# Performance work log

Measured on AMD Instinct MI355X. Metric: run time of the kernel, lower is better.

The kernel has to match this reference:

```python
import jax, jax.numpy as jnp
import numpy as np

B, S, E, H = 2, 2048, 2048, 8
D = E // H          # 256, also PMSNorm width
LAYER_IDX = 3
EPS = 1e-5
NEG = jnp.finfo(jnp.float32).min


def setup_inputs() -> dict:
    key = jax.random.key(0)
    k1, k2, k3 = jax.random.split(key, 3)
    return {
        "hidden_state": jax.random.normal(k1, (B, S, E), dtype=jnp.float32),
        "w_attn": jax.random.normal(k2, (E, 3 * E), dtype=jnp.float32) * 0.02,
        "w_proj": jax.random.normal(k3, (E, E), dtype=jnp.float32) * 0.02,
        "norm_weight": jnp.ones((D,), dtype=jnp.float32),
    }


def reference(hidden_state, w_attn, w_proj, norm_weight):
    # qkv projection (Linear, no bias): [B,S,3E]
    qkv = hidden_state @ w_attn
    q, k, v = jnp.split(qkv, 3, axis=-1)
    # split heads -> [B,H,S,D]
    q = q.reshape(B, S, H, D).transpose(0, 2, 1, 3)
    k = k.reshape(B, S, H, D).transpose(0, 2, 1, 3)
    v = v.reshape(B, S, H, D).transpose(0, 2, 1, 3)
    # scaled scores, extra layer-idx scaling as in the module
    scale = jnp.asarray(D, jnp.float32) ** 0.5 * (LAYER_IDX + 1)
    scores = jnp.einsum("bhqd,bhkd->bhqk", q, k) / scale
    # causal mask (tril buffer): masked positions -> float32 min
    causal = jnp.tril(jnp.ones((S, S), dtype=bool))
    scores = jnp.where(causal[None, None], scores, NEG)
    attn = jax.nn.softmax(scores, axis=-1)  # dropout is identity in eval
    o = jnp.einsum("bhqk,bhkd->bhqd", attn, v)
    # PMSNorm over last dim D (applied per-head, as in the source)
    o = o * jax.lax.rsqrt(jnp.mean(o * o, axis=-1, keepdims=True) + EPS)
    o = o * norm_weight
    # merge heads -> [B,S,E], output projection
    merged = o.transpose(0, 2, 1, 3).reshape(B, S, E)
    return merged @ w_proj
```

## Files before the change

### kernel.cpp

```cpp
#include <hip/hip_runtime.h>
#include <math.h>


typedef unsigned short u16;
typedef unsigned int   u32;
typedef u16   u16x8 __attribute__((ext_vector_type(8)));
typedef __bf16 bf16x8 __attribute__((ext_vector_type(8)));
typedef float f32x4 __attribute__((ext_vector_type(4)));

#define GPTR(p) ((const __attribute__((address_space(1))) void*)(p))
#define LPTR(p) ((__attribute__((address_space(3))) void*)(p))

__device__ __forceinline__ u16 f2bf(float x) {
  u32 u = __float_as_uint(x);
  return (u16)((u + 0x7fffu + ((u >> 16) & 1u)) >> 16);
}

__device__ __forceinline__ bf16x8 ld8(const void* p) {
  u16x8 v = *reinterpret_cast<const u16x8*>(p);
  return __builtin_bit_cast(bf16x8, v);
}

__device__ __forceinline__ void g2l16(const void* g, void* l) {
  __builtin_amdgcn_global_load_lds(GPTR(g), LPTR(l), 16, 0, 0);
}

__global__ void cast_bf16_kernel(const float* __restrict__ in, u16* __restrict__ out, int n8) {
  int i = blockIdx.x * 256 + threadIdx.x;
  if (i >= n8) return;
  const float4* p = reinterpret_cast<const float4*>(in) + (size_t)i * 2;
  float4 a = p[0], b = p[1];
  u16x8 v;
  v[0] = f2bf(a.x); v[1] = f2bf(a.y); v[2] = f2bf(a.z); v[3] = f2bf(a.w);
  v[4] = f2bf(b.x); v[5] = f2bf(b.y); v[6] = f2bf(b.z); v[7] = f2bf(b.w);
  reinterpret_cast<u16x8*>(out)[i] = v;
}

__global__ void tcast_kernel(const float* __restrict__ in, u16* __restrict__ out, int R, int C) {
  __shared__ float t[32][33];
  int bx = blockIdx.x * 32, by = blockIdx.y * 32;
  int x = threadIdx.x, y = threadIdx.y;
  #pragma unroll
  for (int k = 0; k < 32; k += 8)
    t[y + k][x] = in[(size_t)(by + y + k) * C + (bx + x)];
  __syncthreads();
  #pragma unroll
  for (int k = 0; k < 32; k += 8)
    out[(size_t)(bx + y + k) * R + (by + x)] = f2bf(t[x][y + k]);
}

__global__ void tv_kernel(const u16* __restrict__ qkv, u16* __restrict__ out) {
  __shared__ u16 t[32][33];
  int bh = blockIdx.z, b = bh >> 3, h = bh & 7;
  const u16* ip = qkv + (size_t)b * 2048 * 6144 + 4096 + h * 256;
  u16* op = out + (size_t)bh * 256 * 2048;
  int bx = blockIdx.x * 32, by = blockIdx.y * 32;
  int x = threadIdx.x, y = threadIdx.y;
  #pragma unroll
  for (int k = 0; k < 32; k += 8)
    t[y + k][x] = ip[(size_t)(by + y + k) * 6144 + (bx + x)];
  __syncthreads();
  #pragma unroll
  for (int k = 0; k < 32; k += 8)
    op[(size_t)(bx + y + k) * 2048 + (by + x)] = t[x][y + k];
}

__global__ __launch_bounds__(256) void gemm_bt_kernel(
    const u16* __restrict__ A, const u16* __restrict__ Bt,
    float* __restrict__ Cf, u16* __restrict__ Cb, int M, int N, int K) {
  __shared__ __align__(16) u16 sA[128 * 64];
  __shared__ __align__(16) u16 sB[128 * 64];
  const int tid = threadIdx.x;
  const int lane = tid & 63, w = tid >> 6;
  const int wr = w >> 1, wc = w & 1;
  const int g = lane >> 4, li = lane & 15;
  const int bn = blockIdx.x * 128, bm = blockIdx.y * 128;

  const char* aSrc[4]; const char* bSrc[4];
  char* aDst[4]; char* bDst[4];
  #pragma unroll
  for (int j = 0; j < 4; ++j) {
    int chunk = w * 4 + j;
    int o = chunk * 1024 + lane * 16;
    int row = o >> 7, cb = o & 127;
    int cbs = cb ^ ((row & 7) << 4);
    aSrc[j] = (const char*)A + (size_t)(bm + row) * K * 2 + cbs;
    bSrc[j] = (const char*)Bt + (size_t)(bn + row) * K * 2 + cbs;
    aDst[j] = (char*)sA + chunk * 1024;
    bDst[j] = (char*)sB + chunk * 1024;
  }
  const char* aRd[2][4]; const char* bRd[2][4];
  #pragma unroll
  for (int ks = 0; ks < 2; ++ks) {
    #pragma unroll
    for (int f = 0; f < 4; ++f) {
      int ra = wr * 64 + f * 16 + li;
      aRd[ks][f] = (const char*)sA + ra * 128 + ((ks * 64 + g * 16) ^ ((ra & 7) << 4));
      int rb = wc * 64 + f * 16 + li;
      bRd[ks][f] = (const char*)sB + rb * 128 + ((ks * 64 + g * 16) ^ ((rb & 7) << 4));
    }
  }

  const f32x4 fz = {0.f, 0.f, 0.f, 0.f};
  f32x4 acc[4][4];
  #pragma unroll
  for (int i = 0; i < 4; ++i)
    #pragma unroll
    for (int j = 0; j < 4; ++j) acc[i][j] = fz;

  for (int k0 = 0; k0 < K; k0 += 64) {
    #pragma unroll
    for (int j = 0; j < 4; ++j) { g2l16(aSrc[j], aDst[j]); g2l16(bSrc[j], bDst[j]); }
    #pragma unroll
    for (int j = 0; j < 4; ++j) { aSrc[j] += 128; bSrc[j] += 128; }
    __syncthreads();
    bf16x8 af[2][4], bfv[2][4];
    #pragma unroll
    for (int ks = 0; ks < 2; ++ks)
      #pragma unroll
      for (int f = 0; f < 4; ++f) { af[ks][f] = ld8(aRd[ks][f]); bfv[ks][f] = ld8(bRd[ks][f]); }
    #pragma unroll
    for (int ks = 0; ks < 2; ++ks)
      #pragma unroll
      for (int mf = 0; mf < 4; ++mf)
        #pragma unroll
        for (int nf = 0; nf < 4; ++nf)
          acc[mf][nf] = __builtin_amdgcn_mfma_f32_16x16x32_bf16(af[ks][mf], bfv[ks][nf], acc[mf][nf], 0, 0, 0);
    __syncthreads();
  }

  if (Cf) {
    #pragma unroll
    for (int mf = 0; mf < 4; ++mf)
      #pragma unroll
      for (int nf = 0; nf < 4; ++nf)
        #pragma unroll
        for (int r = 0; r < 4; ++r) {
          int gm = bm + wr * 64 + mf * 16 + g * 4 + r;
          int gn = bn + wc * 64 + nf * 16 + li;
          Cf[(size_t)gm * N + gn] = acc[mf][nf][r];
        }
  } else {
    #pragma unroll
    for (int mf = 0; mf < 4; ++mf)
      #pragma unroll
      for (int nf = 0; nf < 4; ++nf)
        #pragma unroll
        for (int r = 0; r < 4; ++r) {
          int gm = bm + wr * 64 + mf * 16 + g * 4 + r;
          int gn = bn + wc * 64 + nf * 16 + li;
          Cb[(size_t)gm * N + gn] = f2bf(acc[mf][nf][r]);
        }
  }
}

__global__ __launch_bounds__(512, 2) void attn_kernel(
    const u16* __restrict__ qkv, const u16* __restrict__ Vt,
    const float* __restrict__ nw, u16* __restrict__ Mrg) {
  __shared__ __align__(16) char smem[106496];
  char* sKb = smem;
  char* sVb = smem + 65536;
  char* sPb = smem + 65536 + 32768;
  float* oex  = (float*)smem;
  float* mlex = (float*)(smem + 65536);

  const int c = blockIdx.x;
  const int bh = c & 15, iu = c >> 4;
  const int b = bh >> 3, h = bh & 7;
  const int tid = threadIdx.x, lane = tid & 63, w = tid >> 6;
  const int kh = w >> 2, wq = w & 3;
  const int g = lane >> 4, li = lane & 15;
  const float MASKV = -30000.0f;
  const float MINIT = -1000.0f;
  const float isc = 1.0f / 64.0f;
  const f32x4 fz = {0.f, 0.f, 0.f, 0.f};
  const size_t KADV = (size_t)32 * 6144 * 2;

  #pragma unroll 1
  for (int uu = 0; uu < 2; ++uu) {
    const int qt = uu ? (31 - iu) : iu;
    const int nt = qt + 1;
    const int kvb0 = kh * nt * 32;

    int qrow = qt * 64 + wq * 16 + li;
    const u16* qp = qkv + (size_t)(b * 2048 + qrow) * 6144 + h * 256;
    bf16x8 qf[8];
    #pragma unroll
    for (int c8 = 0; c8 < 8; ++c8) qf[c8] = ld8(qp + c8 * 32 + g * 8);

    const char* kSrc[4]; u32 kDoff[4];
    #pragma unroll
    for (int j = 0; j < 4; ++j) {
      int chunk = wq * 4 + j;
      int o = chunk * 1024 + lane * 16;
      int row = o >> 9, cb = o & 511;
      int cbs = cb ^ ((row & 7) << 4);
      kSrc[j] = (const char*)qkv + ((size_t)(b * 2048 + kvb0 + row) * 6144 + 2048 + h * 256) * 2 + cbs;
      kDoff[j] = chunk * 1024;
    }
    const char* vSrc[4]; char* vDst[4];
    #pragma unroll
    for (int j = 0; j < 4; ++j) {
      int chunk = wq * 4 + j;
      int o = chunk * 1024 + lane * 16;
      int row = o >> 6, cb = o & 63;
      int cbs = cb ^ (((row >> 1) & 3) << 4);
      vSrc[j] = (const char*)Vt + ((size_t)(bh * 256 + row) * 2048 + kvb0) * 2 + cbs;
      vDst[j] = sVb + kh * 16384 + chunk * 1024;
    }

    f32x4 o_[16];
    #pragma unroll
    for (int nf = 0; nf < 16; ++nf) o_[nf] = fz;
    float m_[4] = {MINIT, MINIT, MINIT, MINIT};
    float l_[4] = {0.f, 0.f, 0.f, 0.f};

    {
      char* kb0 = sKb + (kh * 2 + 0) * 16384;
      #pragma unroll
      for (int j = 0; j < 4; ++j) { g2l16(kSrc[j], kb0 + kDoff[j]); kSrc[j] += KADV; }
    }
    asm volatile("s_waitcnt vmcnt(0)" ::: "memory");
    asm volatile("s_barrier" ::: "memory");

    int cur = 0;
    for (int t = 0; t < nt; ++t) {
      const bool more = (t < nt - 1);
      #pragma unroll
      for (int j = 0; j < 4; ++j) { g2l16(vSrc[j], vDst[j]); vSrc[j] += 64; }
      if (more) {
        char* kb = sKb + (kh * 2 + (cur ^ 1)) * 16384;
        #pragma unroll
        for (int j = 0; j < 4; ++j) { g2l16(kSrc[j], kb + kDoff[j]); kSrc[j] += KADV; }
      }

      f32x4 sacc[2];
      const char* kbase = sKb + (kh * 2 + cur) * 16384;
      __builtin_amdgcn_s_setprio(1);
      #pragma unroll
      for (int nf = 0; nf < 2; ++nf) {
        int row = nf * 16 + li;
        int swz = (row & 7) << 4;
        const char* kr = kbase + row * 512;
        f32x4 sa = fz, sb = fz;
        #pragma unroll
        for (int c8 = 0; c8 < 4; ++c8) {
          sa = __builtin_amdgcn_mfma_f32_16x16x32_bf16(qf[c8],     ld8(kr + ((c8 * 64 + g * 16) ^ swz)),       sa, 0, 0, 0);
          sb = __builtin_amdgcn_mfma_f32_16x16x32_bf16(qf[c8 + 4], ld8(kr + (((c8 + 4) * 64 + g * 16) ^ swz)), sb, 0, 0, 0);
        }
        sacc[nf] = sa + sb;
      }
      __builtin_amdgcn_s_setprio(0);

      const int tidx = kh * nt + t;
      const bool diag = (tidx >= 2 * qt);
      float p[2][4], m0[4];
      #pragma unroll
      for (int r = 0; r < 4; ++r) {
        int qr = qt * 64 + wq * 16 + g * 4 + r;
        float a0 = sacc[0][r] * isc;
        float a1 = sacc[1][r] * isc;
        if (diag) {
          if (tidx * 32 + li > qr) a0 = MASKV;
          if (tidx * 32 + 16 + li > qr) a1 = MASKV;
        }
        p[0][r] = a0; p[1][r] = a1;
        m0[r] = fmaxf(a0, a1);
      }
      bool need = (m0[0] > m_[0] + 8.f) || (m0[1] > m_[1] + 8.f) ||
                  (m0[2] > m_[2] + 8.f) || (m0[3] > m_[3] + 8.f);
      if (__any(need)) {
        #pragma unroll
        for (int r = 0; r < 4; ++r) {
          float mx = m0[r];
          mx = fmaxf(mx, __shfl_xor(mx, 1));
          mx = fmaxf(mx, __shfl_xor(mx, 2));
          mx = fmaxf(mx, __shfl_xor(mx, 4));
          mx = fmaxf(mx, __shfl_xor(mx, 8));
          float mn = fmaxf(m_[r], mx);
          float sc = __expf(m_[r] - mn);
          l_[r] *= sc; m_[r] = mn;
          #pragma unroll
          for (int nf = 0; nf < 16; ++nf) o_[nf][r] *= sc;
        }
      }
      #pragma unroll
      for (int r = 0; r < 4; ++r) {
        float e0 = __expf(p[0][r] - m_[r]);
        float e1 = __expf(p[1][r] - m_[r]);
        p[0][r] = e0; p[1][r] = e1;
        l_[r] += e0 + e1;
      }

      if (more) asm volatile("s_waitcnt vmcnt(4)" ::: "memory");
      else      asm volatile("s_waitcnt vmcnt(0)" ::: "memory");
      asm volatile("s_barrier" ::: "memory");

      char* sPw = sPb + kh * 4096 + wq * 1024;
      #pragma unroll
      for (int r = 0; r < 4; ++r) {
        int row = g * 4 + r;
        int swz = ((row >> 1) & 3) << 4;
        #pragma unroll
        for (int nf = 0; nf < 2; ++nf)
          *(u16*)(sPw + row * 64 + (((nf * 16 + li) * 2) ^ swz)) = f2bf(p[nf][r]);
      }
      asm volatile("s_waitcnt lgkmcnt(0)" ::: "memory");
      __builtin_amdgcn_sched_barrier(0);

      __builtin_amdgcn_s_setprio(1);
      {
        const char* vb = sVb + kh * 16384;
        bf16x8 pa = ld8(sPw + li * 64 + ((g * 16) ^ (((li >> 1) & 3) << 4)));
        #pragma unroll
        for (int nf = 0; nf < 16; ++nf) {
          int row = nf * 16 + li;
          bf16x8 vf = ld8(vb + row * 64 + ((g * 16) ^ (((row >> 1) & 3) << 4)));
          o_[nf] = __builtin_amdgcn_mfma_f32_16x16x32_bf16(pa, vf, o_[nf], 0, 0, 0);
        }
      }
      __builtin_amdgcn_s_setprio(0);

      asm volatile("s_barrier" ::: "memory");
      if (more) asm volatile("s_waitcnt vmcnt(0)" ::: "memory");
      cur ^= 1;
    }

    if (kh == 1) {
      #pragma unroll
      for (int nf = 0; nf < 16; ++nf)
        *(f32x4*)(oex + wq * 4096 + nf * 256 + lane * 4) = o_[nf];
      #pragma unroll
      for (int r = 0; r < 4; ++r) {
        mlex[wq * 512 + r * 64 + lane] = l_[r];
        mlex[wq * 512 + 256 + r * 64 + lane] = m_[r];
      }
    }
    __syncthreads();
    if (kh == 0) {
      float aw[4], bw[4], inv_l[4];
      #pragma unroll
      for (int r = 0; r < 4; ++r) {
        float mB = mlex[wq * 512 + 256 + r * 64 + lane];
        float lB = mlex[wq * 512 + r * 64 + lane];
        float mm = fmaxf(m_[r], mB);
        aw[r] = __expf(m_[r] - mm);
        bw[r] = __expf(mB - mm);
        float lr = l_[r] * aw[r] + lB * bw[r];
        lr += __shfl_xor(lr, 1);
        lr += __shfl_xor(lr, 2);
        lr += __shfl_xor(lr, 4);
        lr += __shfl_xor(lr, 8);
        inv_l[r] = 1.0f / lr;
      }
      #pragma unroll
      for (int nf = 0; nf < 16; ++nf) {
        f32x4 ob = *(f32x4*)(oex + wq * 4096 + nf * 256 + lane * 4);
        #pragma unroll
        for (int r = 0; r < 4; ++r)
          o_[nf][r] = o_[nf][r] * aw[r] + ob[r] * bw[r];
      }
      #pragma unroll
      for (int r = 0; r < 4; ++r) {
        float ss = 0.f;
        #pragma unroll
        for (int nf = 0; nf < 16; ++nf) {
          float v = o_[nf][r] * inv_l[r];
          ss += v * v;
        }
        ss += __shfl_xor(ss, 1);
        ss += __shfl_xor(ss, 2);
        ss += __shfl_xor(ss, 4);
        ss += __shfl_xor(ss, 8);
        float rms = rsqrtf(ss * (1.0f / 256.0f) + 1e-5f);
        int row = qt * 64 + wq * 16 + g * 4 + r;
        #pragma unroll
        for (int nf = 0; nf < 16; ++nf) {
          int d = nf * 16 + li;
          float v = o_[nf][r] * inv_l[r] * rms * nw[d];
          Mrg[((size_t)(b * 2048 + row)) * 2048 + h * 256 + d] = f2bf(v);
        }
      }
    }
    __syncthreads();
  }
}

extern "C" void kernel_launch(void* const* d_in, const int* in_sizes, int n_in,
                              void* d_out, int out_size, void* d_ws, size_t ws_size,
                              hipStream_t stream) {
  const float* hs  = (const float*)d_in[0];
  const float* wat = (const float*)d_in[1];
  const float* wpr = (const float*)d_in[2];
  const float* nw  = (const float*)d_in[3];
  float* out = (float*)d_out;

  char* ws = (char*)d_ws;
  u16* Xb   = (u16*)(ws + 0);
  u16* Wp_t = (u16*)(ws + (16u << 20));
  u16* Qkv  = (u16*)(ws + (24u << 20));
  u16* Vt   = (u16*)(ws + (72u << 20));
  u16* Mrg  = Xb;
  u16* Wa_t = (u16*)d_out;

  dim3 t328(32, 8);
  cast_bf16_kernel<<<4096, 256, 0, stream>>>(hs, Xb, 1048576);
  tcast_kernel<<<dim3(192, 64), t328, 0, stream>>>(wat, Wa_t, 2048, 6144);
  tcast_kernel<<<dim3(64, 64), t328, 0, stream>>>(wpr, Wp_t, 2048, 2048);
  gemm_bt_kernel<<<dim3(48, 32), 256, 0, stream>>>(Xb, Wa_t, nullptr, Qkv, 4096, 6144, 2048);
  tv_kernel<<<dim3(8, 64, 16), t328, 0, stream>>>(Qkv, Vt);
  attn_kernel<<<256, 512, 0, stream>>>(Qkv, Vt, nw, Mrg);
  gemm_bt_kernel<<<dim3(16, 32), 256, 0, stream>>>(Mrg, Wp_t, out, nullptr, 4096, 2048, 2048);
  (void)in_sizes; (void)n_in; (void)out_size; (void)ws_size;
}
```

Measured before the change: 268.9 us.

## Use 256x256 double-buffered GEMM tile for QKV projection

Adds a new GEMM kernel that computes a 256x256 output tile per 512-thread block. It double-buffers the LDS loads issued via global_load_lds, so the next K-slice is fetched while MFMA runs on the current one, and raises wave priority around the MFMA bursts. It replaces the 128x128 kernel for the QKV projection only, to improve data reuse and hide load latency. The cost is 128 KB of LDS per block and 384 blocks on 256 CUs, which gives a partial second wave and possible occupancy limits.

```diff
diff --git a/kernel.cpp b/kernel.cpp
--- a/kernel.cpp
+++ b/kernel.cpp
@@ -63,6 +63,122 @@
   #pragma unroll
   for (int k = 0; k < 32; k += 8)
     op[(size_t)(bx + y + k) * 2048 + (by + x)] = t[x][y + k];
+}
+
+__global__ __launch_bounds__(512, 2) void gemm256_kernel(
+    const u16* __restrict__ A, const u16* __restrict__ Bt,
+    float* __restrict__ Cf, u16* __restrict__ Cb, int M, int N, int K) {
+  __shared__ __align__(16) u16 sA[2][256 * 64];
+  __shared__ __align__(16) u16 sB[2][256 * 64];
+  const int tid = threadIdx.x;
+  const int lane = tid & 63, w = tid >> 6;
+  const int wr = w >> 2, wc = w & 3;
+  const int g = lane >> 4, li = lane & 15;
+  const int bn = blockIdx.x * 256, bm = blockIdx.y * 256;
+
+  const char* aSrc[4]; const char* bSrc[4]; u32 dOff[4];
+  #pragma unroll
+  for (int j = 0; j < 4; ++j) {
+    int chunk = w * 4 + j;
+    int o = chunk * 1024 + lane * 16;
+    int row = o >> 7;
+    int cbs = (o & 127) ^ ((row & 7) << 4);
+    aSrc[j] = (const char*)A + (size_t)(bm + row) * K * 2 + cbs;
+    bSrc[j] = (const char*)Bt + (size_t)(bn + row) * K * 2 + cbs;
+    dOff[j] = (u32)chunk * 1024;
+  }
+
+  const f32x4 fz = {0.f, 0.f, 0.f, 0.f};
+  f32x4 acc[8][4];
+  #pragma unroll
+  for (int i = 0; i < 8; ++i)
+    #pragma unroll
+    for (int j = 0; j < 4; ++j) acc[i][j] = fz;
+
+  const int NT = K >> 6;
+  #pragma unroll
+  for (int j = 0; j < 4; ++j) {
+    g2l16(aSrc[j], (char*)sA[0] + dOff[j]);
+    g2l16(bSrc[j], (char*)sB[0] + dOff[j]);
+    aSrc[j] += 128; bSrc[j] += 128;
+  }
+
+  for (int t = 0; t < NT; ++t) {
+    const int cur = t & 1;
+    const bool more = (t + 1 < NT);
+    asm volatile("s_barrier" ::: "memory");
+    if (more) {
+      #pragma unroll
+      for (int j = 0; j < 4; ++j) {
+        g2l16(aSrc[j], (char*)sA[cur ^ 1] + dOff[j]);
+        g2l16(bSrc[j], (char*)sB[cur ^ 1] + dOff[j]);
+        aSrc[j] += 128; bSrc[j] += 128;
+      }
+      asm volatile("s_waitcnt vmcnt(8)" ::: "memory");
+    } else {
+      asm volatile("s_waitcnt vmcnt(0)" ::: "memory");
+    }
+    asm volatile("s_barrier" ::: "memory");
+
+    const char* sAb = (const char*)sA[cur];
+    const char* sBb = (const char*)sB[cur];
+    bf16x8 bReg[2][4];
+    #pragma unroll
+    for (int nf = 0; nf < 4; ++nf) {
+      int rb = wc * 64 + nf * 16 + li;
+      int swz = (rb & 7) << 4;
+      const char* base = sBb + rb * 128;
+      bReg[0][nf] = ld8(base + ((g * 16) ^ swz));
+      bReg[1][nf] = ld8(base + ((64 + g * 16) ^ swz));
+    }
+    #pragma unroll
+    for (int q = 0; q < 4; ++q) {
+      bf16x8 aReg[2][2];
+      #pragma unroll
+      for (int sub = 0; sub < 2; ++sub) {
+        int ra = wr * 128 + (2 * q + sub) * 16 + li;
+        int swz = (ra & 7) << 4;
+        const char* base = sAb + ra * 128;
+        aReg[0][sub] = ld8(base + ((g * 16) ^ swz));
+        aReg[1][sub] = ld8(base + ((64 + g * 16) ^ swz));
+      }
+      __builtin_amdgcn_s_setprio(1);
+      #pragma unroll
+      for (int sub = 0; sub < 2; ++sub)
+        #pragma unroll
+        for (int nf = 0; nf < 4; ++nf)
+          #pragma unroll
+          for (int ks = 0; ks < 2; ++ks)
+            acc[2 * q + sub][nf] =
+                __builtin_amdgcn_mfma_f32_16x16x32_bf16(aReg[ks][sub], bReg[ks][nf],
+                                                        acc[2 * q + sub][nf], 0, 0, 0);
+      __builtin_amdgcn_s_setprio(0);
+    }
+  }
+
+  if (Cb) {
+    #pragma unroll
+    for (int mf = 0; mf < 8; ++mf)
+      #pragma unroll
+      for (int nf = 0; nf < 4; ++nf)
+        #pragma unroll
+        for (int r = 0; r < 4; ++r) {
+          int gm = bm + wr * 128 + mf * 16 + g * 4 + r;
+          int gn = bn + wc * 64 + nf * 16 + li;
+          Cb[(size_t)gm * N + gn] = f2bf(acc[mf][nf][r]);
+        }
+  } else {
+    #pragma unroll
+    for (int mf = 0; mf < 8; ++mf)
+      #pragma unroll
+      for (int nf = 0; nf < 4; ++nf)
+        #pragma unroll
+        for (int r = 0; r < 4; ++r) {
+          int gm = bm + wr * 128 + mf * 16 + g * 4 + r;
+          int gn = bn + wc * 64 + nf * 16 + li;
+          Cf[(size_t)gm * N + gn] = acc[mf][nf][r];
+        }
+  }
 }
 
 __global__ __launch_bounds__(256) void gemm_bt_kernel(
@@ -407,7 +523,7 @@
   cast_bf16_kernel<<<4096, 256, 0, stream>>>(hs, Xb, 1048576);
   tcast_kernel<<<dim3(192, 64), t328, 0, stream>>>(wat, Wa_t, 2048, 6144);
   tcast_kernel<<<dim3(64, 64), t328, 0, stream>>>(wpr, Wp_t, 2048, 2048);
-  gemm_bt_kernel<<<dim3(48, 32), 256, 0, stream>>>(Xb, Wa_t, nullptr, Qkv, 4096, 6144, 2048);
+  gemm256_kernel<<<dim3(24, 16), 512, 0, stream>>>(Xb, Wa_t, nullptr, Qkv, 4096, 6144, 2048);
   tv_kernel<<<dim3(8, 64, 16), t328, 0, stream>>>(Qkv, Vt);
   attn_kernel<<<256, 512, 0, stream>>>(Qkv, Vt, nw, Mrg);
   gemm_bt_kernel<<<dim3(16, 32), 256, 0, stream>>>(Mrg, Wp_t, out, nullptr, 4096, 2048, 2048);
```

New measurement: 278.6 us. 1.04x slower.

## Replace bf16 GEMM with 8-wave ping-pong pipelined kernel using larger tiles

Applied to the files above, without the earlier changes.

Replaces the simple 128x128 single-buffered GEMM with a templated 512-thread kernel that double-buffers LDS, splits each K-step into half-tiles, and interleaves async global-to-LDS loads with MFMA phases under explicit barriers, waitcnt and setprio. Tiles grow to 256x192 for the QKV projection and 256x128 for the output projection. The goal is to hide global load latency behind matrix math and raise arithmetic intensity. The hand-counted vmcnt values and dense barrier schedule are fragile, and the larger tiles cut the number of blocks.

```diff
diff --git a/kernel.cpp b/kernel.cpp
--- a/kernel.cpp
+++ b/kernel.cpp
@@ -65,93 +65,169 @@
     op[(size_t)(bx + y + k) * 2048 + (by + x)] = t[x][y + k];
 }
 
-__global__ __launch_bounds__(256) void gemm_bt_kernel(
+template<int WM, int WN, int MF, int NF, bool F32OUT>
+__global__ __launch_bounds__(512, 2) void gemm8p_kernel(
     const u16* __restrict__ A, const u16* __restrict__ Bt,
     float* __restrict__ Cf, u16* __restrict__ Cb, int M, int N, int K) {
-  __shared__ __align__(16) u16 sA[128 * 64];
-  __shared__ __align__(16) u16 sB[128 * 64];
-  const int tid = threadIdx.x;
-  const int lane = tid & 63, w = tid >> 6;
-  const int wr = w >> 1, wc = w & 1;
+  constexpr int BM = WM * MF * 16;
+  constexpr int BN = WN * NF * 16;
+  constexpr int BSTG = (BN * 128) / 8192;
+  constexpr int BBYTES = BN * 128;
+  __shared__ __align__(16) char smem[65536 + 2 * BBYTES];
+  char* sAb = smem;
+  char* sBb = smem + 65536;
+
+  const int tid = threadIdx.x, lane = tid & 63, w = tid >> 6;
+  const int wr = w / WN, wc = w % WN;
   const int g = lane >> 4, li = lane & 15;
-  const int bn = blockIdx.x * 128, bm = blockIdx.y * 128;
-
-  const char* aSrc[4]; const char* bSrc[4];
-  char* aDst[4]; char* bDst[4];
-  #pragma unroll
-  for (int j = 0; j < 4; ++j) {
-    int chunk = w * 4 + j;
-    int o = chunk * 1024 + lane * 16;
-    int row = o >> 7, cb = o & 127;
-    int cbs = cb ^ ((row & 7) << 4);
-    aSrc[j] = (const char*)A + (size_t)(bm + row) * K * 2 + cbs;
-    bSrc[j] = (const char*)Bt + (size_t)(bn + row) * K * 2 + cbs;
-    aDst[j] = (char*)sA + chunk * 1024;
-    bDst[j] = (char*)sB + chunk * 1024;
+  const int bn = blockIdx.x * BN, bm = blockIdx.y * BM;
+
+  const char* aS[2][2];
+  #pragma unroll
+  for (int h = 0; h < 2; ++h)
+    #pragma unroll
+    for (int j = 0; j < 2; ++j) {
+      int o = j * 8192 + tid * 16;
+      int row = o >> 6;
+      int col = (o & 63) ^ (((row >> 1) & 3) << 4);
+      aS[h][j] = (const char*)A + (size_t)(bm + row) * K * 2 + h * 64 + col;
+    }
+  const char* bS[BSTG];
+  #pragma unroll
+  for (int j = 0; j < BSTG; ++j) {
+    int o = j * 8192 + tid * 16;
+    int h = o / (BN * 64);
+    int rem = o - h * (BN * 64);
+    int row = rem >> 6;
+    int col = (rem & 63) ^ (((row >> 1) & 3) << 4);
+    bS[j] = (const char*)Bt + (size_t)(bn + row) * K * 2 + h * 64 + col;
   }
-  const char* aRd[2][4]; const char* bRd[2][4];
-  #pragma unroll
-  for (int ks = 0; ks < 2; ++ks) {
-    #pragma unroll
-    for (int f = 0; f < 4; ++f) {
-      int ra = wr * 64 + f * 16 + li;
-      aRd[ks][f] = (const char*)sA + ra * 128 + ((ks * 64 + g * 16) ^ ((ra & 7) << 4));
-      int rb = wc * 64 + f * 16 + li;
-      bRd[ks][f] = (const char*)sB + rb * 128 + ((ks * 64 + g * 16) ^ ((rb & 7) << 4));
-    }
+
+  u32 aRd[MF], bRd[NF];
+  #pragma unroll
+  for (int mf = 0; mf < MF; ++mf) {
+    int row = wr * (MF * 16) + mf * 16 + li;
+    aRd[mf] = row * 64 + ((g * 16) ^ (((row >> 1) & 3) << 4));
   }
+  #pragma unroll
+  for (int nf = 0; nf < NF; ++nf) {
+    int row = wc * (NF * 16) + nf * 16 + li;
+    bRd[nf] = row * 64 + ((g * 16) ^ (((row >> 1) & 3) << 4));
+  }
+
+  auto stageA = [&](int h, int buf) {
+    char* d = sAb + (buf * 2 + h) * 16384 + w * 1024;
+    g2l16(aS[h][0], d);
+    g2l16(aS[h][1], d + 8192);
+    aS[h][0] += 128; aS[h][1] += 128;
+  };
+  auto stageB = [&](int buf) {
+    char* d = sBb + buf * BBYTES + w * 1024;
+    #pragma unroll
+    for (int j = 0; j < BSTG; ++j) { g2l16(bS[j], d + j * 8192); bS[j] += 128; }
+  };
 
   const f32x4 fz = {0.f, 0.f, 0.f, 0.f};
-  f32x4 acc[4][4];
-  #pragma unroll
-  for (int i = 0; i < 4; ++i)
-    #pragma unroll
-    for (int j = 0; j < 4; ++j) acc[i][j] = fz;
-
-  for (int k0 = 0; k0 < K; k0 += 64) {
-    #pragma unroll
-    for (int j = 0; j < 4; ++j) { g2l16(aSrc[j], aDst[j]); g2l16(bSrc[j], bDst[j]); }
-    #pragma unroll
-    for (int j = 0; j < 4; ++j) { aSrc[j] += 128; bSrc[j] += 128; }
-    __syncthreads();
-    bf16x8 af[2][4], bfv[2][4];
-    #pragma unroll
-    for (int ks = 0; ks < 2; ++ks)
-      #pragma unroll
-      for (int f = 0; f < 4; ++f) { af[ks][f] = ld8(aRd[ks][f]); bfv[ks][f] = ld8(bRd[ks][f]); }
-    #pragma unroll
-    for (int ks = 0; ks < 2; ++ks)
-      #pragma unroll
-      for (int mf = 0; mf < 4; ++mf)
-        #pragma unroll
-        for (int nf = 0; nf < 4; ++nf)
-          acc[mf][nf] = __builtin_amdgcn_mfma_f32_16x16x32_bf16(af[ks][mf], bfv[ks][nf], acc[mf][nf], 0, 0, 0);
-    __syncthreads();
+  f32x4 acc[MF][NF];
+  #pragma unroll
+  for (int i = 0; i < MF; ++i)
+    #pragma unroll
+    for (int j = 0; j < NF; ++j) acc[i][j] = fz;
+
+  const int NT = K >> 6;
+
+  stageA(0, 0);
+  stageB(0);
+  stageA(1, 0);
+  stageA(0, 1);
+  asm volatile("s_waitcnt vmcnt(4)" ::: "memory");
+  asm volatile("s_barrier" ::: "memory");
+
+  for (int k = 0; k < NT; ++k) {
+    const int cbuf = k & 1, nbuf = cbuf ^ 1;
+    const bool s1 = (k + 1 < NT), s2 = (k + 2 < NT);
+    const char* sAc = sAb + cbuf * 32768;
+    const char* sBc = sBb + cbuf * BBYTES;
+    bf16x8 aR[MF / 2], bR[NF];
+
+    #pragma unroll
+    for (int i = 0; i < MF / 2; ++i) aR[i] = ld8(sAc + aRd[i]);
+    #pragma unroll
+    for (int nf = 0; nf < NF; ++nf) bR[nf] = ld8(sBc + bRd[nf]);
+    if (s1) { stageA(1, nbuf); stageB(nbuf); }
+    asm volatile("s_barrier" ::: "memory");
+    asm volatile("s_waitcnt lgkmcnt(0)" ::: "memory");
+    __builtin_amdgcn_sched_barrier(0);
+    __builtin_amdgcn_s_setprio(1);
+    #pragma unroll
+    for (int i = 0; i < MF / 2; ++i)
+      #pragma unroll
+      for (int nf = 0; nf < NF; ++nf)
+        acc[i][nf] = __builtin_amdgcn_mfma_f32_16x16x32_bf16(aR[i], bR[nf], acc[i][nf], 0, 0, 0);
+    __builtin_amdgcn_s_setprio(0);
+    asm volatile("s_barrier" ::: "memory");
+
+    #pragma unroll
+    for (int i = 0; i < MF / 2; ++i) aR[i] = ld8(sAc + aRd[MF / 2 + i]);
+    asm volatile("s_barrier" ::: "memory");
+    asm volatile("s_waitcnt lgkmcnt(0)" ::: "memory");
+    __builtin_amdgcn_sched_barrier(0);
+    __builtin_amdgcn_s_setprio(1);
+    #pragma unroll
+    for (int i = 0; i < MF / 2; ++i)
+      #pragma unroll
+      for (int nf = 0; nf < NF; ++nf)
+        acc[MF / 2 + i][nf] = __builtin_amdgcn_mfma_f32_16x16x32_bf16(aR[i], bR[nf], acc[MF / 2 + i][nf], 0, 0, 0);
+    __builtin_amdgcn_s_setprio(0);
+    if (s1) asm volatile("s_waitcnt vmcnt(%0)" :: "i"(4 + BSTG) : "memory");
+    else    asm volatile("s_waitcnt vmcnt(0)" ::: "memory");
+    asm volatile("s_barrier" ::: "memory");
+
+    #pragma unroll
+    for (int i = 0; i < MF / 2; ++i) aR[i] = ld8(sAc + 16384 + aRd[i]);
+    #pragma unroll
+    for (int nf = 0; nf < NF; ++nf) bR[nf] = ld8(sBc + BN * 64 + bRd[nf]);
+    if (s2) stageA(0, cbuf);
+    asm volatile("s_barrier" ::: "memory");
+    asm volatile("s_waitcnt lgkmcnt(0)" ::: "memory");
+    __builtin_amdgcn_sched_barrier(0);
+    __builtin_amdgcn_s_setprio(1);
+    #pragma unroll
+    for (int i = 0; i < MF / 2; ++i)
+      #pragma unroll
+      for (int nf = 0; nf < NF; ++nf)
+        acc[i][nf] = __builtin_amdgcn_mfma_f32_16x16x32_bf16(aR[i], bR[nf], acc[i][nf], 0, 0, 0);
+    __builtin_amdgcn_s_setprio(0);
+    asm volatile("s_barrier" ::: "memory");
+
+    #pragma unroll
+    for (int i = 0; i < MF / 2; ++i) aR[i] = ld8(sAc + 16384 + aRd[MF / 2 + i]);
+    asm volatile("s_barrier" ::: "memory");
+    asm volatile("s_waitcnt lgkmcnt(0)" ::: "memory");
+    __builtin_amdgcn_sched_barrier(0);
+    __builtin_amdgcn_s_setprio(1);
+    #pragma unroll
+    for (int i = 0; i < MF / 2; ++i)
+      #pragma unroll
+      for (int nf = 0; nf < NF; ++nf)
+        acc[MF / 2 + i][nf] = __builtin_amdgcn_mfma_f32_16x16x32_bf16(aR[i], bR[nf], acc[MF / 2 + i][nf], 0, 0, 0);
+    __builtin_amdgcn_s_setprio(0);
+    if (s2) asm volatile("s_waitcnt vmcnt(2)" ::: "memory");
+    else    asm volatile("s_waitcnt vmcnt(0)" ::: "memory");
+    asm volatile("s_barrier" ::: "memory");
   }
 
-  if (Cf) {
-    #pragma unroll
-    for (int mf = 0; mf < 4; ++mf)
-      #pragma unroll
-      for (int nf = 0; nf < 4; ++nf)
-        #pragma unroll
-        for (int r = 0; r < 4; ++r) {
-          int gm = bm + wr * 64 + mf * 16 + g * 4 + r;
-          int gn = bn + wc * 64 + nf * 16 + li;
-          Cf[(size_t)gm * N + gn] = acc[mf][nf][r];
-        }
-  } else {
-    #pragma unroll
-    for (int mf = 0; mf < 4; ++mf)
-      #pragma unroll
-      for (int nf = 0; nf < 4; ++nf)
-        #pragma unroll
-        for (int r = 0; r < 4; ++r) {
-          int gm = bm + wr * 64 + mf * 16 + g * 4 + r;
-          int gn = bn + wc * 64 + nf * 16 + li;
-          Cb[(size_t)gm * N + gn] = f2bf(acc[mf][nf][r]);
-        }
-  }
+  #pragma unroll
+  for (int mf = 0; mf < MF; ++mf)
+    #pragma unroll
+    for (int nf = 0; nf < NF; ++nf)
+      #pragma unroll
+      for (int r = 0; r < 4; ++r) {
+        int gm = bm + wr * (MF * 16) + mf * 16 + g * 4 + r;
+        int gn = bn + wc * (NF * 16) + nf * 16 + li;
+        if (F32OUT) Cf[(size_t)gm * N + gn] = acc[mf][nf][r];
+        else        Cb[(size_t)gm * N + gn] = f2bf(acc[mf][nf][r]);
+      }
 }
 
 __global__ __launch_bounds__(512, 2) void attn_kernel(
@@ -407,9 +483,11 @@
   cast_bf16_kernel<<<4096, 256, 0, stream>>>(hs, Xb, 1048576);
   tcast_kernel<<<dim3(192, 64), t328, 0, stream>>>(wat, Wa_t, 2048, 6144);
   tcast_kernel<<<dim3(64, 64), t328, 0, stream>>>(wpr, Wp_t, 2048, 2048);
-  gemm_bt_kernel<<<dim3(48, 32), 256, 0, stream>>>(Xb, Wa_t, nullptr, Qkv, 4096, 6144, 2048);
+  gemm8p_kernel<2, 4, 8, 3, false><<<dim3(32, 16), 512, 0, stream>>>(
+      Xb, Wa_t, nullptr, Qkv, 4096, 6144, 2048);
   tv_kernel<<<dim3(8, 64, 16), t328, 0, stream>>>(Qkv, Vt);
   attn_kernel<<<256, 512, 0, stream>>>(Qkv, Vt, nw, Mrg);
-  gemm_bt_kernel<<<dim3(16, 32), 256, 0, stream>>>(Mrg, Wp_t, out, nullptr, 4096, 2048, 2048);
+  gemm8p_kernel<4, 2, 4, 4, true><<<dim3(16, 16), 512, 0, stream>>>(
+      Mrg, Wp_t, out, nullptr, 4096, 2048, 2048);
   (void)in_sizes; (void)n_in; (void)out_size; (void)ws_size;
 }
```

Result: faster. 247.7 us (-7.9%).

## Double-buffer GEMM LDS tiles with async loads and templated 512-thread tiles

Applied to the files above, without the earlier changes.

Replaces the single-buffered 256-thread GEMM with a templated 512-thread kernel that double-buffers A/B tiles in LDS. The next tile's global-to-LDS loads are issued before computing on the current one, with explicit vmcnt waits and barriers. MFMA sections are wrapped in s_setprio raises. The tile shapes change: QKV uses 128x192 tiles on a 32x32 grid and the output projection uses 128x128 with 8 waves. More LDS per block and higher register pressure may limit occupancy.

```diff
diff --git a/kernel.cpp b/kernel.cpp
--- a/kernel.cpp
+++ b/kernel.cpp
@@ -65,93 +65,107 @@
     op[(size_t)(bx + y + k) * 2048 + (by + x)] = t[x][y + k];
 }
 
-__global__ __launch_bounds__(256) void gemm_bt_kernel(
+template<int WM, int WN, int MF, int NF, bool F32OUT>
+__global__ __launch_bounds__(512, 4) void gemm2b_kernel(
     const u16* __restrict__ A, const u16* __restrict__ Bt,
     float* __restrict__ Cf, u16* __restrict__ Cb, int M, int N, int K) {
-  __shared__ __align__(16) u16 sA[128 * 64];
-  __shared__ __align__(16) u16 sB[128 * 64];
-  const int tid = threadIdx.x;
-  const int lane = tid & 63, w = tid >> 6;
-  const int wr = w >> 1, wc = w & 1;
+  constexpr int BM = WM * MF * 16;
+  constexpr int BN = WN * NF * 16;
+  constexpr int TILEB = (BM + BN) * 128;
+  constexpr int NSTG = TILEB / 8192;
+  __shared__ __align__(16) char smem[2 * TILEB];
+
+  const int tid = threadIdx.x, lane = tid & 63, w = tid >> 6;
+  const int wr = w / WN, wc = w % WN;
   const int g = lane >> 4, li = lane & 15;
-  const int bn = blockIdx.x * 128, bm = blockIdx.y * 128;
-
-  const char* aSrc[4]; const char* bSrc[4];
-  char* aDst[4]; char* bDst[4];
-  #pragma unroll
-  for (int j = 0; j < 4; ++j) {
-    int chunk = w * 4 + j;
-    int o = chunk * 1024 + lane * 16;
-    int row = o >> 7, cb = o & 127;
-    int cbs = cb ^ ((row & 7) << 4);
-    aSrc[j] = (const char*)A + (size_t)(bm + row) * K * 2 + cbs;
-    bSrc[j] = (const char*)Bt + (size_t)(bn + row) * K * 2 + cbs;
-    aDst[j] = (char*)sA + chunk * 1024;
-    bDst[j] = (char*)sB + chunk * 1024;
+  const int bn = blockIdx.x * BN, bm = blockIdx.y * BM;
+
+  const char* src[NSTG]; u32 dOff[NSTG];
+  #pragma unroll
+  for (int j = 0; j < NSTG; ++j) {
+    int o = j * 8192 + tid * 16;
+    if (o < BM * 128) {
+      int row = o >> 7;
+      int col = (o & 127) ^ ((row & 7) << 4);
+      src[j] = (const char*)A + (size_t)(bm + row) * K * 2 + col;
+    } else {
+      int rem = o - BM * 128;
+      int row = rem >> 7;
+      int col = (rem & 127) ^ ((row & 7) << 4);
+      src[j] = (const char*)Bt + (size_t)(bn + row) * K * 2 + col;
+    }
+    dOff[j] = (u32)(o - lane * 16);
   }
-  const char* aRd[2][4]; const char* bRd[2][4];
+
+  u32 aRd[2][MF], bRd[2][NF];
   #pragma unroll
   for (int ks = 0; ks < 2; ++ks) {
     #pragma unroll
-    for (int f = 0; f < 4; ++f) {
-      int ra = wr * 64 + f * 16 + li;
-      aRd[ks][f] = (const char*)sA + ra * 128 + ((ks * 64 + g * 16) ^ ((ra & 7) << 4));
-      int rb = wc * 64 + f * 16 + li;
-      bRd[ks][f] = (const char*)sB + rb * 128 + ((ks * 64 + g * 16) ^ ((rb & 7) << 4));
+    for (int mf = 0; mf < MF; ++mf) {
+      int row = wr * (MF * 16) + mf * 16 + li;
+      aRd[ks][mf] = row * 128 + ((ks * 64 + g * 16) ^ ((row & 7) << 4));
+    }
+    #pragma unroll
+    for (int nf = 0; nf < NF; ++nf) {
+      int row = wc * (NF * 16) + nf * 16 + li;
+      bRd[ks][nf] = BM * 128 + row * 128 + ((ks * 64 + g * 16) ^ ((row & 7) << 4));
     }
   }
 
   const f32x4 fz = {0.f, 0.f, 0.f, 0.f};
-  f32x4 acc[4][4];
-  #pragma unroll
-  for (int i = 0; i < 4; ++i)
-    #pragma unroll
-    for (int j = 0; j < 4; ++j) acc[i][j] = fz;
-
-  for (int k0 = 0; k0 < K; k0 += 64) {
-    #pragma unroll
-    for (int j = 0; j < 4; ++j) { g2l16(aSrc[j], aDst[j]); g2l16(bSrc[j], bDst[j]); }
-    #pragma unroll
-    for (int j = 0; j < 4; ++j) { aSrc[j] += 128; bSrc[j] += 128; }
-    __syncthreads();
-    bf16x8 af[2][4], bfv[2][4];
-    #pragma unroll
-    for (int ks = 0; ks < 2; ++ks)
-      #pragma unroll
-      for (int f = 0; f < 4; ++f) { af[ks][f] = ld8(aRd[ks][f]); bfv[ks][f] = ld8(bRd[ks][f]); }
-    #pragma unroll
-    for (int ks = 0; ks < 2; ++ks)
-      #pragma unroll
-      for (int mf = 0; mf < 4; ++mf)
-        #pragma unroll
-        for (int nf = 0; nf < 4; ++nf)
-          acc[mf][nf] = __builtin_amdgcn_mfma_f32_16x16x32_bf16(af[ks][mf], bfv[ks][nf], acc[mf][nf], 0, 0, 0);
-    __syncthreads();
+  f32x4 acc[MF][NF];
+  #pragma unroll
+  for (int i = 0; i < MF; ++i)
+    #pragma unroll
+    for (int j = 0; j < NF; ++j) acc[i][j] = fz;
+
+  const int NT = K >> 6;
+  #pragma unroll
+  for (int j = 0; j < NSTG; ++j) { g2l16(src[j], smem + dOff[j]); src[j] += 128; }
+
+  for (int t = 0; t < NT; ++t) {
+    const int cur = t & 1;
+    const bool more = (t + 1 < NT);
+    asm volatile("s_barrier" ::: "memory");
+    if (more) {
+      char* nb = smem + (cur ^ 1) * TILEB;
+      #pragma unroll
+      for (int j = 0; j < NSTG; ++j) { g2l16(src[j], nb + dOff[j]); src[j] += 128; }
+      asm volatile("s_waitcnt vmcnt(%0)" :: "i"(NSTG) : "memory");
+    } else {
+      asm volatile("s_waitcnt vmcnt(0)" ::: "memory");
+    }
+    asm volatile("s_barrier" ::: "memory");
+
+    const char* sb = smem + cur * TILEB;
+    #pragma unroll
+    for (int ks = 0; ks < 2; ++ks) {
+      bf16x8 aR[MF], bR[NF];
+      #pragma unroll
+      for (int mf = 0; mf < MF; ++mf) aR[mf] = ld8(sb + aRd[ks][mf]);
+      #pragma unroll
+      for (int nf = 0; nf < NF; ++nf) bR[nf] = ld8(sb + bRd[ks][nf]);
+      __builtin_amdgcn_s_setprio(1);
+      #pragma unroll
+      for (int mf = 0; mf < MF; ++mf)
+        #pragma unroll
+        for (int nf = 0; nf < NF; ++nf)
+          acc[mf][nf] = __builtin_amdgcn_mfma_f32_16x16x32_bf16(aR[mf], bR[nf], acc[mf][nf], 0, 0, 0);
+      __builtin_amdgcn_s_setprio(0);
+    }
   }
 
-  if (Cf) {
-    #pragma unroll
-    for (int mf = 0; mf < 4; ++mf)
-      #pragma unroll
-      for (int nf = 0; nf < 4; ++nf)
-        #pragma unroll
-        for (int r = 0; r < 4; ++r) {
-          int gm = bm + wr * 64 + mf * 16 + g * 4 + r;
-          int gn = bn + wc * 64 + nf * 16 + li;
-          Cf[(size_t)gm * N + gn] = acc[mf][nf][r];
-        }
-  } else {
-    #pragma unroll
-    for (int mf = 0; mf < 4; ++mf)
-      #pragma unroll
-      for (int nf = 0; nf < 4; ++nf)
-        #pragma unroll
-        for (int r = 0; r < 4; ++r) {
-          int gm = bm + wr * 64 + mf * 16 + g * 4 + r;
-          int gn = bn + wc * 64 + nf * 16 + li;
-          Cb[(size_t)gm * N + gn] = f2bf(acc[mf][nf][r]);
-        }
-  }
+  #pragma unroll
+  for (int mf = 0; mf < MF; ++mf)
+    #pragma unroll
+    for (int nf = 0; nf < NF; ++nf)
+      #pragma unroll
+      for (int r = 0; r < 4; ++r) {
+        int gm = bm + wr * (MF * 16) + mf * 16 + g * 4 + r;
+        int gn = bn + wc * (NF * 16) + nf * 16 + li;
+        if (F32OUT) Cf[(size_t)gm * N + gn] = acc[mf][nf][r];
+        else        Cb[(size_t)gm * N + gn] = f2bf(acc[mf][nf][r]);
+      }
 }
 
 __global__ __launch_bounds__(512, 2) void attn_kernel(
@@ -407,9 +421,11 @@
   cast_bf16_kernel<<<4096, 256, 0, stream>>>(hs, Xb, 1048576);
   tcast_kernel<<<dim3(192, 64), t328, 0, stream>>>(wat, Wa_t, 2048, 6144);
   tcast_kernel<<<dim3(64, 64), t328, 0, stream>>>(wpr, Wp_t, 2048, 2048);
-  gemm_bt_kernel<<<dim3(48, 32), 256, 0, stream>>>(Xb, Wa_t, nullptr, Qkv, 4096, 6144, 2048);
+  gemm2b_kernel<2, 4, 4, 3, false><<<dim3(32, 32), 512, 0, stream>>>(
+      Xb, Wa_t, nullptr, Qkv, 4096, 6144, 2048);
   tv_kernel<<<dim3(8, 64, 16), t328, 0, stream>>>(Qkv, Vt);
   attn_kernel<<<256, 512, 0, stream>>>(Qkv, Vt, nw, Mrg);
-  gemm_bt_kernel<<<dim3(16, 32), 256, 0, stream>>>(Mrg, Wp_t, out, nullptr, 4096, 2048, 2048);
+  gemm2b_kernel<2, 4, 4, 2, true><<<dim3(16, 32), 512, 0, stream>>>(
+      Mrg, Wp_t, out, nullptr, 4096, 2048, 2048);
   (void)in_sizes; (void)n_in; (void)out_size; (void)ws_size;
 }
```

Measured after the change: 237.4 us. 1.13x faster.
